# Kernel tuning notes

Hardware: AMD Instinct MI355X
Metric: run time of the kernel (lower is better)

The kernel has to match this reference:

```python
import jax, jax.numpy as jnp
import numpy as np


def setup_inputs() -> dict:
    key = jax.random.key(0)
    kq, kk = jax.random.split(key)
    B, H, T, D = 4, 12, 2048, 64
    q = jax.random.normal(kq, (B, H, T, D), dtype=jnp.float32)
    k = jax.random.normal(kk, (B, H, T, D), dtype=jnp.float32)
    return {"q": q, "k": k, "T": T, "block_size": T}


def reference(q, k, T, block_size):
    # scaled QK^T: [B,H,T,T]
    scale = k.shape[-1] ** (-0.5)
    scores = jnp.einsum("bhqd,bhkd->bhqk", q, k) * scale
    # causal mask (tril[:T,:T] == 0 -> -inf); T == seq len here
    causal = jnp.tril(jnp.ones((T, T), dtype=bool))
    scores = jnp.where(causal, scores, -jnp.inf)
    # softmax over keys; dropout=0.0 (eval / p=0) is identity
    return jax.nn.softmax(scores, axis=-1)
```

## Files before the change

### kernel.cpp

```cpp
#include <hip/hip_runtime.h>

#define T_DIM 2048
#define D_DIM 64
#define BH 48

typedef _Float16 f16x8 __attribute__((ext_vector_type(8)));
typedef _Float16 f16x4 __attribute__((ext_vector_type(4)));
typedef float f32x4 __attribute__((ext_vector_type(4)));

__global__ void cvt_f32_f16(const float* __restrict__ src, _Float16* __restrict__ dst, int n4) {
    int i = blockIdx.x * blockDim.x + threadIdx.x;
    if (i >= n4) return;
    float4 v = ((const float4* __restrict__)src)[i];
    f16x4 h = { (_Float16)v.x, (_Float16)v.y, (_Float16)v.z, (_Float16)v.w };
    ((f16x4*)dst)[i] = h;
}

__global__ __launch_bounds__(256) void sdp_kernel(const _Float16* __restrict__ q16,
                                                  const _Float16* __restrict__ k16,
                                                  float* __restrict__ out) {
    const int T = T_DIM;
    const float scale = 0.125f;

    int bh   = blockIdx.x >> 4;
    int qblk = blockIdx.x & 15;
    int wave = threadIdx.x >> 6;
    int lane = threadIdx.x & 63;
    int g    = lane >> 4;
    int li   = lane & 15;
    int qbase = qblk * 128 + wave * 32;

    const _Float16* qh = q16 + (size_t)bh * T * D_DIM;
    const _Float16* kh = k16 + (size_t)bh * T * D_DIM;
    float* oh = out + (size_t)bh * T * T;

    f16x8 a_lo[2], a_hi[2];
#pragma unroll
    for (int mt = 0; mt < 2; ++mt) {
        const _Float16* p = qh + (size_t)(qbase + mt * 16 + li) * D_DIM;
        a_lo[mt] = *(const f16x8*)(p + g * 8);
        a_hi[mt] = *(const f16x8*)(p + 32 + g * 8);
    }

    int ktmax = (qbase + 31) >> 4;

    float sum[2][4] = {{0.f,0.f,0.f,0.f},{0.f,0.f,0.f,0.f}};
    for (int kt = 0; kt <= ktmax; ++kt) {
        int c = kt * 16 + li;
        const _Float16* p = kh + (size_t)c * D_DIM;
        f16x8 b_lo = *(const f16x8*)(p + g * 8);
        f16x8 b_hi = *(const f16x8*)(p + 32 + g * 8);
#pragma unroll
        for (int mt = 0; mt < 2; ++mt) {
            f32x4 acc = {0.f, 0.f, 0.f, 0.f};
            acc = __builtin_amdgcn_mfma_f32_16x16x32_f16(a_lo[mt], b_lo, acc, 0, 0, 0);
            acc = __builtin_amdgcn_mfma_f32_16x16x32_f16(a_hi[mt], b_hi, acc, 0, 0, 0);
#pragma unroll
            for (int reg = 0; reg < 4; ++reg) {
                int r = qbase + mt * 16 + g * 4 + reg;
                float e = (c <= r) ? __expf(acc[reg] * scale) : 0.f;
                sum[mt][reg] += e;
            }
        }
    }

    float rinv[2][4];
#pragma unroll
    for (int mt = 0; mt < 2; ++mt)
#pragma unroll
        for (int reg = 0; reg < 4; ++reg) {
            float s = sum[mt][reg];
            s += __shfl_xor(s, 1);
            s += __shfl_xor(s, 2);
            s += __shfl_xor(s, 4);
            s += __shfl_xor(s, 8);
            rinv[mt][reg] = 1.0f / s;
        }

    for (int kt = 0; kt <= ktmax; ++kt) {
        int c = kt * 16 + li;
        const _Float16* p = kh + (size_t)c * D_DIM;
        f16x8 b_lo = *(const f16x8*)(p + g * 8);
        f16x8 b_hi = *(const f16x8*)(p + 32 + g * 8);
#pragma unroll
        for (int mt = 0; mt < 2; ++mt) {
            f32x4 acc = {0.f, 0.f, 0.f, 0.f};
            acc = __builtin_amdgcn_mfma_f32_16x16x32_f16(a_lo[mt], b_lo, acc, 0, 0, 0);
            acc = __builtin_amdgcn_mfma_f32_16x16x32_f16(a_hi[mt], b_hi, acc, 0, 0, 0);
#pragma unroll
            for (int reg = 0; reg < 4; ++reg) {
                int r = qbase + mt * 16 + g * 4 + reg;
                float pv = (c <= r) ? __expf(acc[reg] * scale) * rinv[mt][reg] : 0.f;
                oh[(size_t)r * T + c] = pv;
            }
        }
    }

    int zstart = (ktmax + 1) * 16;
    float4 z = make_float4(0.f, 0.f, 0.f, 0.f);
    for (int rr = 0; rr < 32; ++rr) {
        float* rowp = oh + (size_t)(qbase + rr) * T;
        for (int cc = zstart + lane * 4; cc < T; cc += 256)
            *(float4*)(rowp + cc) = z;
    }
}

extern "C" void kernel_launch(void* const* d_in, const int* in_sizes, int n_in,
                              void* d_out, int out_size, void* d_ws, size_t ws_size,
                              hipStream_t stream) {
    const float* q = (const float*)d_in[0];
    const float* k = (const float*)d_in[1];
    float* out = (float*)d_out;

    _Float16* q16 = (_Float16*)d_ws;
    _Float16* k16 = q16 + (size_t)BH * T_DIM * D_DIM;

    int n  = BH * T_DIM * D_DIM;
    int n4 = n / 4;
    cvt_f32_f16<<<(n4 + 255) / 256, 256, 0, stream>>>(q, q16, n4);
    cvt_f32_f16<<<(n4 + 255) / 256, 256, 0, stream>>>(k, k16, n4);

    sdp_kernel<<<BH * 16, 256, 0, stream>>>(q16, k16, out);
}
```

Baseline: 1.008 ms.

## Fuse conversion and compute one-pass softmax with exps cached in shared memory

Replaces the two f32-to-f16 conversion kernels and the two-pass recompute kernel with a single kernel. Each block handles one 16-row query tile, converts q/k on the fly, and stores the fp16 exponentials in swizzled LDS. It reduces row sums across waves, then writes normalized rows with coalesced stores. It also remaps blocks for XCD locality and pairs light and heavy causal tiles. This removes the second QK^T pass and the scattered stores, at the cost of 64KB of LDS per block (limiting occupancy) and fp16 rounding of the stored probabilities.

```diff
diff --git a/kernel.cpp b/kernel.cpp
--- a/kernel.cpp
+++ b/kernel.cpp
@@ -2,106 +2,116 @@
 
 #define T_DIM 2048
 #define D_DIM 64
-#define BH 48
+#define NHEAD 48
+#define NTILE 128
 
 typedef _Float16 f16x8 __attribute__((ext_vector_type(8)));
 typedef _Float16 f16x4 __attribute__((ext_vector_type(4)));
 typedef float f32x4 __attribute__((ext_vector_type(4)));
 
-__global__ void cvt_f32_f16(const float* __restrict__ src, _Float16* __restrict__ dst, int n4) {
-    int i = blockIdx.x * blockDim.x + threadIdx.x;
-    if (i >= n4) return;
-    float4 v = ((const float4* __restrict__)src)[i];
-    f16x4 h = { (_Float16)v.x, (_Float16)v.y, (_Float16)v.z, (_Float16)v.w };
-    ((f16x4*)dst)[i] = h;
+__device__ inline f16x8 cvt8(f32x4 a, f32x4 b) {
+    f16x8 r;
+    r[0] = (_Float16)a[0]; r[1] = (_Float16)a[1];
+    r[2] = (_Float16)a[2]; r[3] = (_Float16)a[3];
+    r[4] = (_Float16)b[0]; r[5] = (_Float16)b[1];
+    r[6] = (_Float16)b[2]; r[7] = (_Float16)b[3];
+    return r;
 }
 
-__global__ __launch_bounds__(256) void sdp_kernel(const _Float16* __restrict__ q16,
-                                                  const _Float16* __restrict__ k16,
-                                                  float* __restrict__ out) {
-    const int T = T_DIM;
+__global__ __launch_bounds__(256) void sdp_onepass(const float* __restrict__ qf,
+                                                   const float* __restrict__ kf,
+                                                   float* __restrict__ out) {
+    __shared__ _Float16 ebuf[16 * T_DIM];
+    __shared__ float sums[4][16];
+
     const float scale = 0.125f;
 
-    int bh   = blockIdx.x >> 4;
-    int qblk = blockIdx.x & 15;
+    int bid  = blockIdx.x;
+    int xcd  = bid & 7;
+    int t    = bid >> 3;
+    int head = xcd + 8 * (t >> 7);
+    int slot = t & 127;
+    int mtg  = (slot & 1) ? (NTILE - 1 - (slot >> 1)) : (slot >> 1);
+
     int wave = threadIdx.x >> 6;
     int lane = threadIdx.x & 63;
     int g    = lane >> 4;
     int li   = lane & 15;
-    int qbase = qblk * 128 + wave * 32;
 
-    const _Float16* qh = q16 + (size_t)bh * T * D_DIM;
-    const _Float16* kh = k16 + (size_t)bh * T * D_DIM;
-    float* oh = out + (size_t)bh * T * T;
+    const float* qh = qf + (size_t)head * T_DIM * D_DIM;
+    const float* kh = kf + (size_t)head * T_DIM * D_DIM;
+    float* oh = out + (size_t)head * T_DIM * T_DIM;
 
-    f16x8 a_lo[2], a_hi[2];
-#pragma unroll
-    for (int mt = 0; mt < 2; ++mt) {
-        const _Float16* p = qh + (size_t)(qbase + mt * 16 + li) * D_DIM;
-        a_lo[mt] = *(const f16x8*)(p + g * 8);
-        a_hi[mt] = *(const f16x8*)(p + 32 + g * 8);
+    const int row0 = mtg * 16;
+    const int NT   = mtg + 1;
+    const int zstart = NT * 16;
+
+    f16x8 b_lo, b_hi;
+    {
+        const float* p = qh + (size_t)(row0 + li) * D_DIM + g * 8;
+        b_lo = cvt8(*(const f32x4*)p,        *(const f32x4*)(p + 4));
+        b_hi = cvt8(*(const f32x4*)(p + 32), *(const f32x4*)(p + 36));
     }
 
-    int ktmax = (qbase + 31) >> 4;
+    float psum = 0.f;
+    const int swz = (li & 7) << 3;
+#pragma unroll 2
+    for (int kt = wave; kt < NT; kt += 4) {
+        const float* p = kh + (size_t)(kt * 16 + li) * D_DIM + g * 8;
+        f16x8 a_lo = cvt8(*(const f32x4*)p,        *(const f32x4*)(p + 4));
+        f16x8 a_hi = cvt8(*(const f32x4*)(p + 32), *(const f32x4*)(p + 36));
 
-    float sum[2][4] = {{0.f,0.f,0.f,0.f},{0.f,0.f,0.f,0.f}};
-    for (int kt = 0; kt <= ktmax; ++kt) {
-        int c = kt * 16 + li;
-        const _Float16* p = kh + (size_t)c * D_DIM;
-        f16x8 b_lo = *(const f16x8*)(p + g * 8);
-        f16x8 b_hi = *(const f16x8*)(p + 32 + g * 8);
+        f32x4 acc = {0.f, 0.f, 0.f, 0.f};
+        acc = __builtin_amdgcn_mfma_f32_16x16x32_f16(a_lo, b_lo, acc, 0, 0, 0);
+        acc = __builtin_amdgcn_mfma_f32_16x16x32_f16(a_hi, b_hi, acc, 0, 0, 0);
+
+        bool diag = (kt == NT - 1);
+        int d = li - g * 4;
+        f16x4 ev;
 #pragma unroll
-        for (int mt = 0; mt < 2; ++mt) {
-            f32x4 acc = {0.f, 0.f, 0.f, 0.f};
-            acc = __builtin_amdgcn_mfma_f32_16x16x32_f16(a_lo[mt], b_lo, acc, 0, 0, 0);
-            acc = __builtin_amdgcn_mfma_f32_16x16x32_f16(a_hi[mt], b_hi, acc, 0, 0, 0);
+        for (int e = 0; e < 4; ++e) {
+            float ex = __expf(acc[e] * scale);
+            if (diag && e > d) ex = 0.f;
+            psum += ex;
+            ev[e] = (_Float16)ex;
+        }
+        int cb = kt * 32 + g * 8;
+        *(f16x4*)((char*)ebuf + li * 4096 + (cb ^ swz)) = ev;
+    }
+
+    {
+        f32x4 z = {0.f, 0.f, 0.f, 0.f};
 #pragma unroll
-            for (int reg = 0; reg < 4; ++reg) {
-                int r = qbase + mt * 16 + g * 4 + reg;
-                float e = (c <= r) ? __expf(acc[reg] * scale) : 0.f;
-                sum[mt][reg] += e;
-            }
+        for (int j = 0; j < 4; ++j) {
+            float* rowp = oh + (size_t)(row0 + wave * 4 + j) * T_DIM;
+            for (int c = zstart + lane * 4; c < T_DIM; c += 256)
+                *(f32x4*)(rowp + c) = z;
         }
     }
 
-    float rinv[2][4];
+    psum += __shfl_xor(psum, 16);
+    psum += __shfl_xor(psum, 32);
+    if (g == 0) sums[wave][li] = psum;
+
+    __syncthreads();
+
+    const int niter = (zstart + 255) >> 8;
 #pragma unroll
-    for (int mt = 0; mt < 2; ++mt)
-#pragma unroll
-        for (int reg = 0; reg < 4; ++reg) {
-            float s = sum[mt][reg];
-            s += __shfl_xor(s, 1);
-            s += __shfl_xor(s, 2);
-            s += __shfl_xor(s, 4);
-            s += __shfl_xor(s, 8);
-            rinv[mt][reg] = 1.0f / s;
-        }
-
-    for (int kt = 0; kt <= ktmax; ++kt) {
-        int c = kt * 16 + li;
-        const _Float16* p = kh + (size_t)c * D_DIM;
-        f16x8 b_lo = *(const f16x8*)(p + g * 8);
-        f16x8 b_hi = *(const f16x8*)(p + 32 + g * 8);
-#pragma unroll
-        for (int mt = 0; mt < 2; ++mt) {
-            f32x4 acc = {0.f, 0.f, 0.f, 0.f};
-            acc = __builtin_amdgcn_mfma_f32_16x16x32_f16(a_lo[mt], b_lo, acc, 0, 0, 0);
-            acc = __builtin_amdgcn_mfma_f32_16x16x32_f16(a_hi[mt], b_hi, acc, 0, 0, 0);
-#pragma unroll
-            for (int reg = 0; reg < 4; ++reg) {
-                int r = qbase + mt * 16 + g * 4 + reg;
-                float pv = (c <= r) ? __expf(acc[reg] * scale) * rinv[mt][reg] : 0.f;
-                oh[(size_t)r * T + c] = pv;
+    for (int j = 0; j < 4; ++j) {
+        int r = wave * 4 + j;
+        float rs = sums[0][r] + sums[1][r] + sums[2][r] + sums[3][r];
+        float rinv = 1.0f / rs;
+        float* rowp = oh + (size_t)(row0 + r) * T_DIM;
+        int rsw = (r & 7) << 3;
+        for (int i = 0; i < niter; ++i) {
+            int col = i * 256 + lane * 4;
+            if (col < zstart) {
+                f16x4 ev = *(const f16x4*)((const char*)ebuf + r * 4096 + ((col * 2) ^ rsw));
+                f32x4 o = { (float)ev[0] * rinv, (float)ev[1] * rinv,
+                            (float)ev[2] * rinv, (float)ev[3] * rinv };
+                *(f32x4*)(rowp + col) = o;
             }
         }
-    }
-
-    int zstart = (ktmax + 1) * 16;
-    float4 z = make_float4(0.f, 0.f, 0.f, 0.f);
-    for (int rr = 0; rr < 32; ++rr) {
-        float* rowp = oh + (size_t)(qbase + rr) * T;
-        for (int cc = zstart + lane * 4; cc < T; cc += 256)
-            *(float4*)(rowp + cc) = z;
     }
 }
 
@@ -111,14 +121,7 @@
     const float* q = (const float*)d_in[0];
     const float* k = (const float*)d_in[1];
     float* out = (float*)d_out;
+    (void)d_ws; (void)ws_size;
 
-    _Float16* q16 = (_Float16*)d_ws;
-    _Float16* k16 = q16 + (size_t)BH * T_DIM * D_DIM;
-
-    int n  = BH * T_DIM * D_DIM;
-    int n4 = n / 4;
-    cvt_f32_f16<<<(n4 + 255) / 256, 256, 0, stream>>>(q, q16, n4);
-    cvt_f32_f16<<<(n4 + 255) / 256, 256, 0, stream>>>(k, k16, n4);
-
-    sdp_kernel<<<BH * 16, 256, 0, stream>>>(q16, k16, out);
+    sdp_onepass<<<NHEAD * NTILE, 256, 0, stream>>>(q, k, out);
 }
```

After: 1.029 ms. 1.02x slower.
